# Kernel tuning notes

Hardware: AMD Instinct MI355X
Metric: run time of the kernel (lower is better)

Reference implementation:

```python
import jax, jax.numpy as jnp
import numpy as np

TEMPERATURE = 0.07
BALANCE = 1.0


def _l2norm(x, eps=1e-12):
    return x / jnp.maximum(jnp.linalg.norm(x, axis=1, keepdims=True), eps)


def setup_inputs() -> dict:
    key = jax.random.key(0)
    k1, k2 = jax.random.split(key)
    B, K, D = 32768, 8192, 384
    features = _l2norm(jax.random.normal(k1, (B, D), dtype=jnp.float32))
    centroids = jax.random.normal(k2, (K, D), dtype=jnp.float32)
    return {"features": features, "centroids": centroids}


def reference(features, centroids):
    # centroids: [K, D] learnable; features: [B, D] sampled batch (L2-normalized)
    c = _l2norm(centroids)
    # chunked matmul + exp + row-max in source == single fused GEMM+exp+max here
    prod_exp = jnp.exp(jnp.matmul(features, c.T) / TEMPERATURE)  # [B, K]
    pos_k = jnp.argmax(prod_exp, axis=1)                          # [B] int
    prod_exp_pos = jnp.max(prod_exp, axis=1)                      # [B]
    # centroid-centroid similarity; first operand is detached in source
    cent_exp = jnp.exp(jnp.matmul(jax.lax.stop_gradient(c), c.T) / TEMPERATURE)  # [K, K]
    cent_sum = jnp.sum(cent_exp, axis=0)                          # [K]
    J = jnp.log(prod_exp_pos) - jnp.log(prod_exp_pos + cent_sum[pos_k] * BALANCE)
    return -jnp.mean(J)
```

## Files before the change

kernel.cpp:

```cpp
#include <hip/hip_runtime.h>
#include <math.h>

constexpr int B = 32768;
constexpr int K = 8192;
constexpr int D = 384;
constexpr float INV_T = 1.0f / 0.07f;

constexpr int TILE_B = 24 * 64 * 16;

typedef int    int8v    __attribute__((ext_vector_type(8)));
typedef float  floatx16 __attribute__((ext_vector_type(16)));

__global__ __launch_bounds__(64) void normalize_k(const float* __restrict__ cent,
                                                  unsigned char* __restrict__ cbs) {
    const int row = blockIdx.x, lane = threadIdx.x;
    const float* src = cent + (size_t)row * D;
    float4 x = {0.f, 0.f, 0.f, 0.f}, y = {0.f, 0.f, 0.f, 0.f};
    if (lane < 48) {
        x = *(const float4*)(src + lane * 8);
        y = *(const float4*)(src + lane * 8 + 4);
    }
    float ss = x.x * x.x + x.y * x.y + x.z * x.z + x.w * x.w
             + y.x * y.x + y.y * y.y + y.z * y.z + y.w * y.w;
#pragma unroll
    for (int off = 32; off > 0; off >>= 1) ss += __shfl_down(ss, off, 64);
    ss = __shfl(ss, 0, 64);
    const float inv = 1.0f / fmaxf(sqrtf(ss), 1e-12f);
    if (lane < 48) {
        int w0 = __builtin_amdgcn_cvt_pk_fp8_f32(x.x * inv, x.y * inv, 0, false);
        w0 = __builtin_amdgcn_cvt_pk_fp8_f32(x.z * inv, x.w * inv, w0, true);
        int w1 = __builtin_amdgcn_cvt_pk_fp8_f32(y.x * inv, y.y * inv, 0, false);
        w1 = __builtin_amdgcn_cvt_pk_fp8_f32(y.z * inv, y.w * inv, w1, true);
        char* dst = (char*)cbs + (size_t)(row >> 6) * TILE_B
                  + ((size_t)(lane >> 1) * 64 + (row & 63)) * 16 + (lane & 1) * 8;
        *(int2*)dst = make_int2(w0, w1);
    }
}

__device__ __forceinline__ void stage_tile_async(const char* __restrict__ gtile,
                                                 char* __restrict__ bs,
                                                 int wave, int lane) {
    const char* g = gtile + wave * 6144 + lane * 16;
    char* l = bs + wave * 6144;
#pragma unroll
    for (int i = 0; i < 6; ++i) {
        __builtin_amdgcn_global_load_lds(
            (const __attribute__((address_space(1))) unsigned int*)(g + i * 1024),
            (__attribute__((address_space(3))) unsigned int*)(l + i * 1024),
            16, 0, 0);
    }
}

__device__ __forceinline__ int8v read_frag(const char* base, int t, int half) {
    const uint4 b0 = *(const uint4*)(base + (4 * t + 2 * half) * 1024);
    const uint4 b1 = *(const uint4*)(base + (4 * t + 2 * half + 1) * 1024);
    int8v f;
    f[0] = b0.x; f[1] = b0.y; f[2] = b0.z; f[3] = b0.w;
    f[4] = b1.x; f[5] = b1.y; f[6] = b1.z; f[7] = b1.w;
    return f;
}

__global__ __launch_bounds__(256, 2) void centsum_k(const unsigned char* __restrict__ cbs,
                                                    float* __restrict__ cent_sum) {
    __shared__ char bs[2][TILE_B];
    const int tid = threadIdx.x, lane = tid & 63, wave = tid >> 6;
    const int wm = wave >> 1, wn = wave & 1;
    const int l31 = lane & 31, half = lane >> 5;
    const int rb = blockIdx.x >> 3, ch = blockIdx.x & 7;

    const int stag = (rb & 3) * 4;
    auto tile_of = [&](int it) { return ch * 16 + ((stag + it) & 15); };

    stage_tile_async((const char*)cbs + (size_t)tile_of(0) * TILE_B, bs[0], wave, lane);

    int8v afr[2][6];
#pragma unroll
    for (int s = 0; s < 2; ++s) {
        const char* abase = (const char*)cbs + (size_t)(rb * 2 + wm) * TILE_B
                          + (s * 32 + l31) * 16;
#pragma unroll
        for (int t = 0; t < 6; ++t) afr[s][t] = read_frag(abase, t, half);
    }

    float rs[2][16];
#pragma unroll
    for (int s = 0; s < 2; ++s)
#pragma unroll
        for (int r = 0; r < 16; ++r) rs[s][r] = 0.f;

    int cur = 0;
    for (int it = 0; it < 16; ++it) {
        __syncthreads();
        if (it + 1 < 16)
            stage_tile_async((const char*)cbs + (size_t)tile_of(it + 1) * TILE_B,
                             bs[cur ^ 1], wave, lane);
        floatx16 acc0, acc1;
#pragma unroll
        for (int r = 0; r < 16; ++r) { acc0[r] = 0.f; acc1[r] = 0.f; }
        const char* bbase = bs[cur] + (wn * 32 + l31) * 16;
#pragma unroll
        for (int t = 0; t < 6; ++t) {
            const int8v bfr = read_frag(bbase, t, half);
            acc0 = __builtin_amdgcn_mfma_scale_f32_32x32x64_f8f6f4(
                       afr[0][t], bfr, acc0, 0, 0, 0, 127, 0, 127);
            acc1 = __builtin_amdgcn_mfma_scale_f32_32x32x64_f8f6f4(
                       afr[1][t], bfr, acc1, 0, 0, 0, 127, 0, 127);
        }
#pragma unroll
        for (int r = 0; r < 16; ++r) {
            rs[0][r] += __expf(acc0[r] * INV_T);
            rs[1][r] += __expf(acc1[r] * INV_T);
        }
        cur ^= 1;
    }

#pragma unroll
    for (int s = 0; s < 2; ++s)
#pragma unroll
        for (int r = 0; r < 16; ++r) {
            float v = rs[s][r];
#pragma unroll
            for (int off = 1; off < 32; off <<= 1) v += __shfl_xor(v, off, 64);
            if (l31 == 0) {
                const int rowl = (r & 3) + 8 * (r >> 2) + 4 * half;
                atomicAdd(&cent_sum[rb * 128 + wm * 64 + s * 32 + rowl], v);
            }
        }
}

__global__ __launch_bounds__(256, 2) void rowmax_k(const float* __restrict__ f,
                                                   const unsigned char* __restrict__ cbs,
                                                   float* __restrict__ row_max2,
                                                   int* __restrict__ row_arg2) {
    __shared__ char bs[2][TILE_B];
    const int tid = threadIdx.x, lane = tid & 63, wave = tid >> 6;
    const int wm = wave >> 1, wn = wave & 1;
    const int l31 = lane & 31, half = lane >> 5;
    const int rb = blockIdx.x >> 1, ch = blockIdx.x & 1;

    const int stag = (rb & 7) * 8;
    auto tile_of = [&](int it) { return ch * 64 + ((stag + it) & 63); };

    stage_tile_async((const char*)cbs + (size_t)tile_of(0) * TILE_B, bs[0], wave, lane);

    int8v afr[2][6];
    const int rowbase = rb * 128 + wm * 64;
#pragma unroll
    for (int s = 0; s < 2; ++s) {
        const float* arow = f + (size_t)(rowbase + s * 32 + l31) * D;
#pragma unroll
        for (int t = 0; t < 6; ++t) {
            const float* p = arow + t * 64 + half * 32;
            int8v a;
#pragma unroll
            for (int q = 0; q < 8; ++q) {
                const float4 v = *(const float4*)(p + q * 4);
                int w = __builtin_amdgcn_cvt_pk_fp8_f32(v.x, v.y, 0, false);
                w = __builtin_amdgcn_cvt_pk_fp8_f32(v.z, v.w, w, true);
                a[q] = w;
            }
            afr[s][t] = a;
        }
    }

    float bv[2][16];
    int   bi[2][16];
#pragma unroll
    for (int s = 0; s < 2; ++s)
#pragma unroll
        for (int r = 0; r < 16; ++r) { bv[s][r] = -INFINITY; bi[s][r] = 0; }

    int cur = 0;
    for (int it = 0; it < 64; ++it) {
        __syncthreads();
        if (it + 1 < 64)
            stage_tile_async((const char*)cbs + (size_t)tile_of(it + 1) * TILE_B,
                             bs[cur ^ 1], wave, lane);
        floatx16 acc0, acc1;
#pragma unroll
        for (int r = 0; r < 16; ++r) { acc0[r] = 0.f; acc1[r] = 0.f; }
        const char* bbase = bs[cur] + (wn * 32 + l31) * 16;
#pragma unroll
        for (int t = 0; t < 6; ++t) {
            const int8v bfr = read_frag(bbase, t, half);
            acc0 = __builtin_amdgcn_mfma_scale_f32_32x32x64_f8f6f4(
                       afr[0][t], bfr, acc0, 0, 0, 0, 127, 0, 127);
            acc1 = __builtin_amdgcn_mfma_scale_f32_32x32x64_f8f6f4(
                       afr[1][t], bfr, acc1, 0, 0, 0, 127, 0, 127);
        }
        const int curCol = tile_of(it) * 64 + wn * 32 + l31;
#pragma unroll
        for (int r = 0; r < 16; ++r) {
            if (acc0[r] > bv[0][r]) { bv[0][r] = acc0[r]; bi[0][r] = curCol; }
            if (acc1[r] > bv[1][r]) { bv[1][r] = acc1[r]; bi[1][r] = curCol; }
        }
        cur ^= 1;
    }

#pragma unroll
    for (int s = 0; s < 2; ++s)
#pragma unroll
        for (int r = 0; r < 16; ++r) {
            float v = bv[s][r]; int ix = bi[s][r];
#pragma unroll
            for (int off = 1; off < 32; off <<= 1) {
                const float ov = __shfl_xor(v, off, 64);
                const int   oi = __shfl_xor(ix, off, 64);
                if (ov > v || (ov == v && oi < ix)) { v = ov; ix = oi; }
            }
            bv[s][r] = v; bi[s][r] = ix;
        }

    __syncthreads();
    float* rv = (float*)bs;
    int*   ri = (int*)bs + 256;
    if (l31 == 0) {
#pragma unroll
        for (int s = 0; s < 2; ++s)
#pragma unroll
            for (int r = 0; r < 16; ++r) {
                const int row = wm * 64 + s * 32 + (r & 3) + 8 * (r >> 2) + 4 * half;
                rv[row * 2 + wn] = bv[s][r];
                ri[row * 2 + wn] = bi[s][r];
            }
    }
    __syncthreads();
    if (tid < 128) {
        const float v0 = rv[tid * 2], v1 = rv[tid * 2 + 1];
        const int   i0 = ri[tid * 2], i1 = ri[tid * 2 + 1];
        const bool take1 = (v1 > v0) || (v1 == v0 && i1 < i0);
        row_max2[(size_t)(rb * 128 + tid) * 2 + ch] = take1 ? v1 : v0;
        row_arg2[(size_t)(rb * 128 + tid) * 2 + ch] = take1 ? i1 : i0;
    }
}

__global__ __launch_bounds__(256) void loss_k(const float* __restrict__ row_max2,
                                              const int* __restrict__ row_arg2,
                                              const float* __restrict__ cent_sum,
                                              float* __restrict__ out) {
    __shared__ float red[256];
    const int tid = threadIdx.x;
    float s = 0.f;
    for (int b = blockIdx.x * 256 + tid; b < B; b += gridDim.x * 256) {
        const float m0 = row_max2[(size_t)b * 2], m1 = row_max2[(size_t)b * 2 + 1];
        const bool take1 = m1 > m0;
        const float m = take1 ? m1 : m0;
        const int ix = row_arg2[(size_t)b * 2 + (take1 ? 1 : 0)];
        s += log1pf(cent_sum[ix] * expf(-m * INV_T));
    }
    red[tid] = s;
    __syncthreads();
    for (int off = 128; off > 0; off >>= 1) {
        if (tid < off) red[tid] += red[tid + off];
        __syncthreads();
    }
    if (tid == 0) atomicAdd(out, red[0] / (float)B);
}

extern "C" void kernel_launch(void* const* d_in, const int* in_sizes, int n_in,
                              void* d_out, int out_size, void* d_ws, size_t ws_size,
                              hipStream_t stream) {
    const float* features  = (const float*)d_in[0];
    const float* centroids = (const float*)d_in[1];
    float* out = (float*)d_out;

    char* ws = (char*)d_ws;
    unsigned char* cbs = (unsigned char*)ws;
    float* cent_sum = (float*)(ws + (size_t)(K / 64) * TILE_B);
    float* row_max2 = cent_sum + K;
    int*   row_arg2 = (int*)(row_max2 + 2 * B);

    hipMemsetAsync(cent_sum, 0, K * sizeof(float), stream);
    hipMemsetAsync(out, 0, sizeof(float), stream);
    normalize_k<<<K, 64, 0, stream>>>(centroids, cbs);
    centsum_k<<<(K / 128) * 8, 256, 0, stream>>>(cbs, cent_sum);
    rowmax_k<<<(B / 128) * 2, 256, 0, stream>>>(features, cbs, row_max2, row_arg2);
    loss_k<<<64, 256, 0, stream>>>(row_max2, row_arg2, cent_sum, out);
}
```

Baseline: 235.4 us.

## Load B fragments directly from global memory instead of LDS double buffering

Both GEMM kernels now drop the async global-to-LDS double-buffered staging and its per-iteration barriers. Each wave reads its B fragments straight from global memory into registers, and the loop is unrolled by two so loads can overlap the MFMAs. The aim is to remove LDS traffic and __syncthreads stalls, relying on L2 to serve the B tiles that waves share. The trade-off is that each tile is fetched from global or cache once per wave rather than once per block, and register pressure rises.

```diff
diff --git a/kernel.cpp b/kernel.cpp
--- a/kernel.cpp
+++ b/kernel.cpp
@@ -37,20 +37,6 @@
     }
 }
 
-__device__ __forceinline__ void stage_tile_async(const char* __restrict__ gtile,
-                                                 char* __restrict__ bs,
-                                                 int wave, int lane) {
-    const char* g = gtile + wave * 6144 + lane * 16;
-    char* l = bs + wave * 6144;
-#pragma unroll
-    for (int i = 0; i < 6; ++i) {
-        __builtin_amdgcn_global_load_lds(
-            (const __attribute__((address_space(1))) unsigned int*)(g + i * 1024),
-            (__attribute__((address_space(3))) unsigned int*)(l + i * 1024),
-            16, 0, 0);
-    }
-}
-
 __device__ __forceinline__ int8v read_frag(const char* base, int t, int half) {
     const uint4 b0 = *(const uint4*)(base + (4 * t + 2 * half) * 1024);
     const uint4 b1 = *(const uint4*)(base + (4 * t + 2 * half + 1) * 1024);
@@ -62,16 +48,11 @@
 
 __global__ __launch_bounds__(256, 2) void centsum_k(const unsigned char* __restrict__ cbs,
                                                     float* __restrict__ cent_sum) {
-    __shared__ char bs[2][TILE_B];
     const int tid = threadIdx.x, lane = tid & 63, wave = tid >> 6;
     const int wm = wave >> 1, wn = wave & 1;
     const int l31 = lane & 31, half = lane >> 5;
     const int rb = blockIdx.x >> 3, ch = blockIdx.x & 7;
-
     const int stag = (rb & 3) * 4;
-    auto tile_of = [&](int it) { return ch * 16 + ((stag + it) & 15); };
-
-    stage_tile_async((const char*)cbs + (size_t)tile_of(0) * TILE_B, bs[0], wave, lane);
 
     int8v afr[2][6];
 #pragma unroll
@@ -88,30 +69,29 @@
 #pragma unroll
         for (int r = 0; r < 16; ++r) rs[s][r] = 0.f;
 
-    int cur = 0;
+#pragma unroll 2
     for (int it = 0; it < 16; ++it) {
-        __syncthreads();
-        if (it + 1 < 16)
-            stage_tile_async((const char*)cbs + (size_t)tile_of(it + 1) * TILE_B,
-                             bs[cur ^ 1], wave, lane);
+        const int tile = ch * 16 + ((stag + it) & 15);
+        const char* gb = (const char*)cbs + (size_t)tile * TILE_B
+                       + (wn * 32 + l31) * 16;
+        int8v bfr[6];
+#pragma unroll
+        for (int t = 0; t < 6; ++t) bfr[t] = read_frag(gb, t, half);
         floatx16 acc0, acc1;
 #pragma unroll
         for (int r = 0; r < 16; ++r) { acc0[r] = 0.f; acc1[r] = 0.f; }
-        const char* bbase = bs[cur] + (wn * 32 + l31) * 16;
 #pragma unroll
         for (int t = 0; t < 6; ++t) {
-            const int8v bfr = read_frag(bbase, t, half);
             acc0 = __builtin_amdgcn_mfma_scale_f32_32x32x64_f8f6f4(
-                       afr[0][t], bfr, acc0, 0, 0, 0, 127, 0, 127);
+                       afr[0][t], bfr[t], acc0, 0, 0, 0, 127, 0, 127);
             acc1 = __builtin_amdgcn_mfma_scale_f32_32x32x64_f8f6f4(
-                       afr[1][t], bfr, acc1, 0, 0, 0, 127, 0, 127);
+                       afr[1][t], bfr[t], acc1, 0, 0, 0, 127, 0, 127);
         }
 #pragma unroll
         for (int r = 0; r < 16; ++r) {
             rs[0][r] += __expf(acc0[r] * INV_T);
             rs[1][r] += __expf(acc1[r] * INV_T);
         }
-        cur ^= 1;
     }
 
 #pragma unroll
@@ -132,16 +112,13 @@
                                                    const unsigned char* __restrict__ cbs,
                                                    float* __restrict__ row_max2,
                                                    int* __restrict__ row_arg2) {
-    __shared__ char bs[2][TILE_B];
+    __shared__ float rv[128 * 2];
+    __shared__ int   ri[128 * 2];
     const int tid = threadIdx.x, lane = tid & 63, wave = tid >> 6;
     const int wm = wave >> 1, wn = wave & 1;
     const int l31 = lane & 31, half = lane >> 5;
     const int rb = blockIdx.x >> 1, ch = blockIdx.x & 1;
-
     const int stag = (rb & 7) * 8;
-    auto tile_of = [&](int it) { return ch * 64 + ((stag + it) & 63); };
-
-    stage_tile_async((const char*)cbs + (size_t)tile_of(0) * TILE_B, bs[0], wave, lane);
 
     int8v afr[2][6];
     const int rowbase = rb * 128 + wm * 64;
@@ -170,31 +147,30 @@
 #pragma unroll
         for (int r = 0; r < 16; ++r) { bv[s][r] = -INFINITY; bi[s][r] = 0; }
 
-    int cur = 0;
+#pragma unroll 2
     for (int it = 0; it < 64; ++it) {
-        __syncthreads();
-        if (it + 1 < 64)
-            stage_tile_async((const char*)cbs + (size_t)tile_of(it + 1) * TILE_B,
-                             bs[cur ^ 1], wave, lane);
+        const int tile = ch * 64 + ((stag + it) & 63);
+        const char* gb = (const char*)cbs + (size_t)tile * TILE_B
+                       + (wn * 32 + l31) * 16;
+        int8v bfr[6];
+#pragma unroll
+        for (int t = 0; t < 6; ++t) bfr[t] = read_frag(gb, t, half);
         floatx16 acc0, acc1;
 #pragma unroll
         for (int r = 0; r < 16; ++r) { acc0[r] = 0.f; acc1[r] = 0.f; }
-        const char* bbase = bs[cur] + (wn * 32 + l31) * 16;
 #pragma unroll
         for (int t = 0; t < 6; ++t) {
-            const int8v bfr = read_frag(bbase, t, half);
             acc0 = __builtin_amdgcn_mfma_scale_f32_32x32x64_f8f6f4(
-                       afr[0][t], bfr, acc0, 0, 0, 0, 127, 0, 127);
+                       afr[0][t], bfr[t], acc0, 0, 0, 0, 127, 0, 127);
             acc1 = __builtin_amdgcn_mfma_scale_f32_32x32x64_f8f6f4(
-                       afr[1][t], bfr, acc1, 0, 0, 0, 127, 0, 127);
-        }
-        const int curCol = tile_of(it) * 64 + wn * 32 + l31;
+                       afr[1][t], bfr[t], acc1, 0, 0, 0, 127, 0, 127);
+        }
+        const int curCol = tile * 64 + wn * 32 + l31;
 #pragma unroll
         for (int r = 0; r < 16; ++r) {
             if (acc0[r] > bv[0][r]) { bv[0][r] = acc0[r]; bi[0][r] = curCol; }
             if (acc1[r] > bv[1][r]) { bv[1][r] = acc1[r]; bi[1][r] = curCol; }
         }
-        cur ^= 1;
     }
 
 #pragma unroll
@@ -211,9 +187,6 @@
             bv[s][r] = v; bi[s][r] = ix;
         }
 
-    __syncthreads();
-    float* rv = (float*)bs;
-    int*   ri = (int*)bs + 256;
     if (l31 == 0) {
 #pragma unroll
         for (int s = 0; s < 2; ++s)
```

Result: slower. 240.5 us (+2.2%).
